# Kernel tuning notes

Hardware: AMD Instinct MI355X
Metric: run time of the kernel (lower is better)

Reference implementation:

```python
import jax, jax.numpy as jnp
import numpy as np

N_NODES = 100000
N_EDGES = 640000
D_FEAT = 128
IN_DIM = 4 + 2 * D_FEAT  # 260
HID = 128
OUT = 128


def setup_inputs() -> dict:
    key = jax.random.key(0)
    ks = jax.random.split(key, 6)
    x = jax.random.normal(ks[0], (N_NODES, D_FEAT), dtype=jnp.float32)
    edge_attr = jax.random.normal(ks[1], (N_EDGES, 4), dtype=jnp.float32)
    edge_index = jax.random.randint(ks[2], (2, N_EDGES), 0, N_NODES, dtype=jnp.int64)
    W1 = jax.random.normal(ks[3], (IN_DIM, HID), dtype=jnp.float32) * (1.0 / np.sqrt(IN_DIM))
    b1 = jnp.zeros((HID,), dtype=jnp.float32)
    W2 = jax.random.normal(ks[4], (HID, OUT), dtype=jnp.float32) * (1.0 / np.sqrt(HID))
    b2 = jnp.zeros((OUT,), dtype=jnp.float32)
    return {"x": x, "edge_attr": edge_attr, "edge_index": edge_index,
            "W1": W1, "b1": b1, "W2": W2, "b2": b2}


def reference(x, edge_attr, edge_index, W1, b1, W2, b2):
    # Gather sender/receiver node features via edge_index: [E, D]
    sender = x[edge_index[0]]
    receiver = x[edge_index[1]]
    # edge_attr already has 4 columns (matches the size-4 check in the torch code)
    edge_inputs = jnp.concatenate([edge_attr, sender, receiver], axis=1)  # [E, 4+2D]
    h = jax.nn.relu(edge_inputs @ W1 + b1)  # [E, HID]
    edge_attr_new = h @ W2 + b2             # [E, OUT]
    return edge_attr_new
```

## Files before the change

### kernel.cpp

```cpp
#include <hip/hip_runtime.h>
#include <hip/hip_bf16.h>

typedef __attribute__((ext_vector_type(4))) float f32x4;
typedef __attribute__((ext_vector_type(8))) short bf16x8;

typedef __attribute__((address_space(1))) unsigned int g_u32;
typedef __attribute__((address_space(3))) unsigned int l_u32;

__device__ __forceinline__ unsigned short f2bf(float f) {
  union { float f; unsigned int u; } v; v.f = f;
  unsigned int u = v.u;
  unsigned int r = (u + 0x7FFFu + ((u >> 16) & 1u)) >> 16;
  return (unsigned short)r;
}

__global__ void pack_w_kernel(const float* __restrict__ W1, const float* __restrict__ W2,
                              unsigned short* __restrict__ Bp1, unsigned short* __restrict__ Bp2) {
  int p = blockIdx.x * 256 + threadIdx.x;
  if (p < 32768) {
    int j = p & 7, n = (p >> 3) & 127, kb = p >> 10;
    Bp1[p] = f2bf(W1[(4 + kb * 8 + j) * 128 + n]);
  } else if (p < 49152) {
    int q = p - 32768;
    int j = q & 7, n = (q >> 3) & 127, kb = q >> 10;
    Bp2[q] = f2bf(W2[(kb * 8 + j) * 128 + n]);
  }
}

__global__ void convert_x_kernel(const float* __restrict__ x, unsigned short* __restrict__ xb, int n8) {
  int i = blockIdx.x * blockDim.x + threadIdx.x;
  if (i >= n8) return;
  const float4* s = (const float4*)x + (size_t)i * 2;
  float4 a = s[0], b = s[1];
  unsigned short h[8] = {f2bf(a.x), f2bf(a.y), f2bf(a.z), f2bf(a.w),
                         f2bf(b.x), f2bf(b.y), f2bf(b.z), f2bf(b.w)};
  int4 pk; __builtin_memcpy(&pk, h, 16);
  ((int4*)xb)[i] = pk;
}

constexpr int BM = 64;

template <bool XBF>
__global__ __launch_bounds__(256, 3)
void edge_main(const float* __restrict__ xf, const unsigned short* __restrict__ xb,
               const float* __restrict__ ea, const int* __restrict__ eidx,
               const float* __restrict__ W1, const float* __restrict__ b1,
               const float* __restrict__ b2,
               const unsigned short* __restrict__ Bp1, const unsigned short* __restrict__ Bp2,
               float* __restrict__ outp, int E) {
  __shared__ int4 AldsV[2048];
  __shared__ int4 HldsV[1024];
  __shared__ float ealds[256];

  char* Alds = (char*)AldsV;
  char* Hlds = (char*)HldsV;

  const int tid  = threadIdx.x;
  const int lane = tid & 63;
  const int wq   = lane >> 4;
  const int l16  = lane & 15;
  const int wave = tid >> 6;
  const int eb   = blockIdx.x * BM;

  ealds[tid] = ea[eb * 4 + tid];

  const int g  = tid & 15;
  const int s0 = tid >> 4;

  int idxv[8];
  #pragma unroll
  for (int it = 0; it < 8; ++it) {
    int seg = it * 16 + s0;
    idxv[it] = eidx[(seg & 1) * E + eb + (seg >> 1)];
  }

  const int c0 = wave * 32 + l16;
  const int c1 = c0 + 16;

  const float bias0 = b1[c0], bias1 = b1[c1];
  const float w00 = W1[c0],       w01 = W1[128 + c0], w02 = W1[256 + c0], w03 = W1[384 + c0];
  const float w10 = W1[c1],       w11 = W1[128 + c1], w12 = W1[256 + c1], w13 = W1[384 + c1];
  const float bias20 = b2[c0], bias21 = b2[c1];

  bf16x8 bf1r[8][2];
  #pragma unroll
  for (int ks = 0; ks < 8; ++ks) {
    int kb = ks * 4 + wq;
    bf1r[ks][0] = __builtin_bit_cast(bf16x8, *(const int4*)(Bp1 + ((size_t)kb * 128 + c0) * 8));
    bf1r[ks][1] = __builtin_bit_cast(bf16x8, *(const int4*)(Bp1 + ((size_t)kb * 128 + c1) * 8));
  }

  if (XBF) {
    #pragma unroll
    for (int it = 0; it < 8; ++it) {
      int seg = it * 16 + s0;
      int r = seg >> 1;
      int gs = g ^ (r & 7);
      const unsigned short* src = xb + (size_t)idxv[it] * 128 + gs * 8;
      char* dstbase = Alds + (it * 16 + wave * 4) * 256;
      __builtin_amdgcn_global_load_lds((g_u32*)(void*)src, (l_u32*)(void*)dstbase, 16, 0, 0);
    }
  } else {
    #pragma unroll
    for (int it = 0; it < 8; ++it) {
      int seg = it * 16 + s0;
      int r = seg >> 1, half = seg & 1;
      int idx = idxv[it];
      int lofs = (r * 512 + half * 256 + g * 16) ^ ((r & 7) << 4);
      const float* src = xf + (size_t)idx * 128 + g * 8;
      float4 a = *(const float4*)src;
      float4 c = *(const float4*)(src + 4);
      unsigned short h[8] = {f2bf(a.x), f2bf(a.y), f2bf(a.z), f2bf(a.w),
                             f2bf(c.x), f2bf(c.y), f2bf(c.z), f2bf(c.w)};
      int4 pk; __builtin_memcpy(&pk, h, 16);
      *(int4*)(Alds + lofs) = pk;
    }
  }
  __syncthreads();

  f32x4 acc[4][2];
  #pragma unroll
  for (int mf = 0; mf < 4; ++mf)
    #pragma unroll
    for (int rg = 0; rg < 4; ++rg) {
      int r = mf * 16 + wq * 4 + rg;
      float e0 = ealds[r * 4 + 0], e1 = ealds[r * 4 + 1];
      float e2 = ealds[r * 4 + 2], e3 = ealds[r * 4 + 3];
      acc[mf][0][rg] = bias0 + e0 * w00 + e1 * w01 + e2 * w02 + e3 * w03;
      acc[mf][1][rg] = bias1 + e0 * w10 + e1 * w11 + e2 * w12 + e3 * w13;
    }

  #pragma unroll
  for (int ks = 0; ks < 8; ++ks) {
    #pragma unroll
    for (int mf = 0; mf < 4; ++mf) {
      int r = mf * 16 + l16;
      int lofs = (r * 512 + ks * 64 + wq * 16) ^ ((r & 7) << 4);
      bf16x8 av = __builtin_bit_cast(bf16x8, *(const int4*)(Alds + lofs));
      acc[mf][0] = __builtin_amdgcn_mfma_f32_16x16x32_bf16(av, bf1r[ks][0], acc[mf][0], 0, 0, 0);
      acc[mf][1] = __builtin_amdgcn_mfma_f32_16x16x32_bf16(av, bf1r[ks][1], acc[mf][1], 0, 0, 0);
    }
  }

  bf16x8 bf2r[4][2];
  #pragma unroll
  for (int ks = 0; ks < 4; ++ks) {
    int kb = ks * 4 + wq;
    bf2r[ks][0] = __builtin_bit_cast(bf16x8, *(const int4*)(Bp2 + ((size_t)kb * 128 + c0) * 8));
    bf2r[ks][1] = __builtin_bit_cast(bf16x8, *(const int4*)(Bp2 + ((size_t)kb * 128 + c1) * 8));
  }

  #pragma unroll
  for (int mf = 0; mf < 4; ++mf)
    #pragma unroll
    for (int nf = 0; nf < 2; ++nf) {
      int c = wave * 32 + nf * 16 + l16;
      #pragma unroll
      for (int rg = 0; rg < 4; ++rg) {
        int r = mf * 16 + wq * 4 + rg;
        float v = fmaxf(acc[mf][nf][rg], 0.0f);
        int lofs = (r * 256 + c * 2) ^ ((r & 7) << 4);
        *(unsigned short*)(Hlds + lofs) = f2bf(v);
      }
    }
  __syncthreads();

  f32x4 acc2[4][2];
  #pragma unroll
  for (int mf = 0; mf < 4; ++mf) {
    acc2[mf][0] = (f32x4){bias20, bias20, bias20, bias20};
    acc2[mf][1] = (f32x4){bias21, bias21, bias21, bias21};
  }
  #pragma unroll
  for (int ks = 0; ks < 4; ++ks) {
    #pragma unroll
    for (int mf = 0; mf < 4; ++mf) {
      int r = mf * 16 + l16;
      int lofs = (r * 256 + ks * 64 + wq * 16) ^ ((r & 7) << 4);
      bf16x8 av = __builtin_bit_cast(bf16x8, *(const int4*)(Hlds + lofs));
      acc2[mf][0] = __builtin_amdgcn_mfma_f32_16x16x32_bf16(av, bf2r[ks][0], acc2[mf][0], 0, 0, 0);
      acc2[mf][1] = __builtin_amdgcn_mfma_f32_16x16x32_bf16(av, bf2r[ks][1], acc2[mf][1], 0, 0, 0);
    }
  }

  #pragma unroll
  for (int mf = 0; mf < 4; ++mf)
    #pragma unroll
    for (int nf = 0; nf < 2; ++nf) {
      int c = wave * 32 + nf * 16 + l16;
      #pragma unroll
      for (int rg = 0; rg < 4; ++rg) {
        int r = mf * 16 + wq * 4 + rg;
        outp[(size_t)(eb + r) * 128 + c] = acc2[mf][nf][rg];
      }
    }
}

extern "C" void kernel_launch(void* const* d_in, const int* in_sizes, int n_in,
                              void* d_out, int out_size, void* d_ws, size_t ws_size,
                              hipStream_t stream) {
  const float* x  = (const float*)d_in[0];
  const float* ea = (const float*)d_in[1];
  const int* eidx = (const int*)d_in[2];
  const float* W1 = (const float*)d_in[3];
  const float* b1 = (const float*)d_in[4];
  const float* W2 = (const float*)d_in[5];
  const float* b2 = (const float*)d_in[6];
  float* outp = (float*)d_out;

  const int E = in_sizes[2] / 2;
  const int nnodes = in_sizes[0] / 128;

  unsigned short* Bp1 = (unsigned short*)d_ws;
  unsigned short* Bp2 = Bp1 + 32768;
  unsigned short* xb  = (unsigned short*)((char*)d_ws + 98304);
  const size_t need = 98304 + (size_t)nnodes * 128 * 2;

  pack_w_kernel<<<192, 256, 0, stream>>>(W1, W2, Bp1, Bp2);

  if (ws_size >= need) {
    int n8 = nnodes * 128 / 8;
    convert_x_kernel<<<(n8 + 255) / 256, 256, 0, stream>>>(x, xb, n8);
    edge_main<true><<<E / BM, 256, 0, stream>>>(x, xb, ea, eidx, W1, b1, b2, Bp1, Bp2, outp, E);
  } else {
    edge_main<false><<<E / BM, 256, 0, stream>>>(x, xb, ea, eidx, W1, b1, b2, Bp1, Bp2, outp, E);
  }
}
```

Before: 156.5 us.

## Make edge MLP kernel persistent with prefetch of next tile's gather

Replaces the one-block-per-tile launch with a persistent grid of up to 768 blocks that loop over edge tiles. Each block keeps its W1 fragments in registers across tiles. It also issues the next tile's index loads, edge_attr loads and async global-to-LDS gathers while the current tile's second GEMM runs. Output stores become nontemporal. The aim is to hide gather latency and amortize per-block weight loading, at the cost of extra barriers and of LDS reuse that relies on explicit waitcnt ordering.

```diff
diff --git a/kernel.cpp b/kernel.cpp
--- a/kernel.cpp
+++ b/kernel.cpp
@@ -40,18 +40,192 @@
 
 constexpr int BM = 64;
 
-template <bool XBF>
 __global__ __launch_bounds__(256, 3)
-void edge_main(const float* __restrict__ xf, const unsigned short* __restrict__ xb,
-               const float* __restrict__ ea, const int* __restrict__ eidx,
-               const float* __restrict__ W1, const float* __restrict__ b1,
-               const float* __restrict__ b2,
-               const unsigned short* __restrict__ Bp1, const unsigned short* __restrict__ Bp2,
-               float* __restrict__ outp, int E) {
+void edge_persist(const unsigned short* __restrict__ xb,
+                  const float* __restrict__ ea, const int* __restrict__ eidx,
+                  const float* __restrict__ W1, const float* __restrict__ b1,
+                  const float* __restrict__ b2,
+                  const unsigned short* __restrict__ Bp1, const unsigned short* __restrict__ Bp2,
+                  float* __restrict__ outp, int E, int ntiles) {
+  __shared__ int4 AldsV[2048];
+  __shared__ int4 HldsV[1024];
+  __shared__ float ealds[2][256];
+
+  char* Alds = (char*)AldsV;
+  char* Hlds = (char*)HldsV;
+
+  const int tid  = threadIdx.x;
+  const int lane = tid & 63;
+  const int wq   = lane >> 4;
+  const int l16  = lane & 15;
+  const int wave = tid >> 6;
+  const int g    = tid & 15;
+  const int s0   = tid >> 4;
+
+  const int c0 = wave * 32 + l16;
+  const int c1 = c0 + 16;
+
+  const float bias0 = b1[c0], bias1 = b1[c1];
+  const float w00 = W1[c0],       w01 = W1[128 + c0], w02 = W1[256 + c0], w03 = W1[384 + c0];
+  const float w10 = W1[c1],       w11 = W1[128 + c1], w12 = W1[256 + c1], w13 = W1[384 + c1];
+  const float bias20 = b2[c0], bias21 = b2[c1];
+
+  bf16x8 bf1r[8][2];
+  #pragma unroll
+  for (int ks = 0; ks < 8; ++ks) {
+    int kb = ks * 4 + wq;
+    bf1r[ks][0] = __builtin_bit_cast(bf16x8, *(const int4*)(Bp1 + ((size_t)kb * 128 + c0) * 8));
+    bf1r[ks][1] = __builtin_bit_cast(bf16x8, *(const int4*)(Bp1 + ((size_t)kb * 128 + c1) * 8));
+  }
+
+  int tile = blockIdx.x;
+  if (tile >= ntiles) return;
+
+  {
+    int idx0[8];
+    #pragma unroll
+    for (int it = 0; it < 8; ++it) {
+      int seg = it * 16 + s0;
+      idx0[it] = eidx[(seg & 1) * E + tile * BM + (seg >> 1)];
+    }
+    ealds[0][tid] = ea[tile * 256 + tid];
+    #pragma unroll
+    for (int it = 0; it < 8; ++it) {
+      int seg = it * 16 + s0;
+      int r = seg >> 1;
+      int gs = g ^ (r & 7);
+      const unsigned short* src = xb + (size_t)idx0[it] * 128 + gs * 8;
+      char* dstbase = Alds + (it * 16 + wave * 4) * 256;
+      __builtin_amdgcn_global_load_lds((g_u32*)(void*)src, (l_u32*)(void*)dstbase, 16, 0, 0);
+    }
+  }
+
+  int p = 0;
+  for (; tile < ntiles; tile += gridDim.x) {
+    const int nt_ = tile + gridDim.x;
+    const int eb  = tile * BM;
+
+    asm volatile("s_waitcnt vmcnt(0) lgkmcnt(0)" ::: "memory");
+    __builtin_amdgcn_s_barrier();
+
+    int idxn[8];
+    if (nt_ < ntiles) {
+      #pragma unroll
+      for (int it = 0; it < 8; ++it) {
+        int seg = it * 16 + s0;
+        idxn[it] = eidx[(seg & 1) * E + nt_ * BM + (seg >> 1)];
+      }
+      ealds[p ^ 1][tid] = ea[nt_ * 256 + tid];
+    }
+
+    f32x4 acc[4][2];
+    #pragma unroll
+    for (int mf = 0; mf < 4; ++mf)
+      #pragma unroll
+      for (int rg = 0; rg < 4; ++rg) {
+        int r = mf * 16 + wq * 4 + rg;
+        float e0 = ealds[p][r * 4 + 0], e1 = ealds[p][r * 4 + 1];
+        float e2 = ealds[p][r * 4 + 2], e3 = ealds[p][r * 4 + 3];
+        acc[mf][0][rg] = bias0 + e0 * w00 + e1 * w01 + e2 * w02 + e3 * w03;
+        acc[mf][1][rg] = bias1 + e0 * w10 + e1 * w11 + e2 * w12 + e3 * w13;
+      }
+
+    #pragma unroll
+    for (int ks = 0; ks < 8; ++ks) {
+      #pragma unroll
+      for (int mf = 0; mf < 4; ++mf) {
+        int r = mf * 16 + l16;
+        int lofs = (r * 512 + ks * 64 + wq * 16) ^ ((r & 7) << 4);
+        bf16x8 av = __builtin_bit_cast(bf16x8, *(const int4*)(Alds + lofs));
+        acc[mf][0] = __builtin_amdgcn_mfma_f32_16x16x32_bf16(av, bf1r[ks][0], acc[mf][0], 0, 0, 0);
+        acc[mf][1] = __builtin_amdgcn_mfma_f32_16x16x32_bf16(av, bf1r[ks][1], acc[mf][1], 0, 0, 0);
+      }
+    }
+
+    asm volatile("s_waitcnt lgkmcnt(0)" ::: "memory");
+    __builtin_amdgcn_s_barrier();
+
+    if (nt_ < ntiles) {
+      #pragma unroll
+      for (int it = 0; it < 8; ++it) {
+        int seg = it * 16 + s0;
+        int r = seg >> 1;
+        int gs = g ^ (r & 7);
+        const unsigned short* src = xb + (size_t)idxn[it] * 128 + gs * 8;
+        char* dstbase = Alds + (it * 16 + wave * 4) * 256;
+        __builtin_amdgcn_global_load_lds((g_u32*)(void*)src, (l_u32*)(void*)dstbase, 16, 0, 0);
+      }
+    }
+
+    bf16x8 bf2r[4][2];
+    #pragma unroll
+    for (int ks = 0; ks < 4; ++ks) {
+      int kb = ks * 4 + wq;
+      bf2r[ks][0] = __builtin_bit_cast(bf16x8, *(const int4*)(Bp2 + ((size_t)kb * 128 + c0) * 8));
+      bf2r[ks][1] = __builtin_bit_cast(bf16x8, *(const int4*)(Bp2 + ((size_t)kb * 128 + c1) * 8));
+    }
+
+    #pragma unroll
+    for (int mf = 0; mf < 4; ++mf)
+      #pragma unroll
+      for (int nf = 0; nf < 2; ++nf) {
+        int c = wave * 32 + nf * 16 + l16;
+        #pragma unroll
+        for (int rg = 0; rg < 4; ++rg) {
+          int r = mf * 16 + wq * 4 + rg;
+          float v = fmaxf(acc[mf][nf][rg], 0.0f);
+          int lofs = (r * 256 + c * 2) ^ ((r & 7) << 4);
+          *(unsigned short*)(Hlds + lofs) = f2bf(v);
+        }
+      }
+
+    asm volatile("s_waitcnt lgkmcnt(0)" ::: "memory");
+    __builtin_amdgcn_s_barrier();
+
+    f32x4 acc2[4][2];
+    #pragma unroll
+    for (int mf = 0; mf < 4; ++mf) {
+      acc2[mf][0] = (f32x4){bias20, bias20, bias20, bias20};
+      acc2[mf][1] = (f32x4){bias21, bias21, bias21, bias21};
+    }
+    #pragma unroll
+    for (int ks = 0; ks < 4; ++ks) {
+      #pragma unroll
+      for (int mf = 0; mf < 4; ++mf) {
+        int r = mf * 16 + l16;
+        int lofs = (r * 256 + ks * 64 + wq * 16) ^ ((r & 7) << 4);
+        bf16x8 av = __builtin_bit_cast(bf16x8, *(const int4*)(Hlds + lofs));
+        acc2[mf][0] = __builtin_amdgcn_mfma_f32_16x16x32_bf16(av, bf2r[ks][0], acc2[mf][0], 0, 0, 0);
+        acc2[mf][1] = __builtin_amdgcn_mfma_f32_16x16x32_bf16(av, bf2r[ks][1], acc2[mf][1], 0, 0, 0);
+      }
+    }
+
+    #pragma unroll
+    for (int mf = 0; mf < 4; ++mf)
+      #pragma unroll
+      for (int nf = 0; nf < 2; ++nf) {
+        int c = wave * 32 + nf * 16 + l16;
+        #pragma unroll
+        for (int rg = 0; rg < 4; ++rg) {
+          int r = mf * 16 + wq * 4 + rg;
+          __builtin_nontemporal_store(acc2[mf][nf][rg], &outp[(size_t)(eb + r) * 128 + c]);
+        }
+      }
+
+    p ^= 1;
+  }
+}
+
+__global__ __launch_bounds__(256, 3)
+void edge_main_f32(const float* __restrict__ xf,
+                   const float* __restrict__ ea, const int* __restrict__ eidx,
+                   const float* __restrict__ W1, const float* __restrict__ b1,
+                   const float* __restrict__ b2,
+                   const unsigned short* __restrict__ Bp1, const unsigned short* __restrict__ Bp2,
+                   float* __restrict__ outp, int E) {
   __shared__ int4 AldsV[2048];
   __shared__ int4 HldsV[1024];
   __shared__ float ealds[256];
-
   char* Alds = (char*)AldsV;
   char* Hlds = (char*)HldsV;
 
@@ -76,7 +250,6 @@
 
   const int c0 = wave * 32 + l16;
   const int c1 = c0 + 16;
-
   const float bias0 = b1[c0], bias1 = b1[c1];
   const float w00 = W1[c0],       w01 = W1[128 + c0], w02 = W1[256 + c0], w03 = W1[384 + c0];
   const float w10 = W1[c1],       w11 = W1[128 + c1], w12 = W1[256 + c1], w13 = W1[384 + c1];
@@ -90,31 +263,18 @@
     bf1r[ks][1] = __builtin_bit_cast(bf16x8, *(const int4*)(Bp1 + ((size_t)kb * 128 + c1) * 8));
   }
 
-  if (XBF) {
-    #pragma unroll
-    for (int it = 0; it < 8; ++it) {
-      int seg = it * 16 + s0;
-      int r = seg >> 1;
-      int gs = g ^ (r & 7);
-      const unsigned short* src = xb + (size_t)idxv[it] * 128 + gs * 8;
-      char* dstbase = Alds + (it * 16 + wave * 4) * 256;
-      __builtin_amdgcn_global_load_lds((g_u32*)(void*)src, (l_u32*)(void*)dstbase, 16, 0, 0);
-    }
-  } else {
-    #pragma unroll
-    for (int it = 0; it < 8; ++it) {
-      int seg = it * 16 + s0;
-      int r = seg >> 1, half = seg & 1;
-      int idx = idxv[it];
-      int lofs = (r * 512 + half * 256 + g * 16) ^ ((r & 7) << 4);
-      const float* src = xf + (size_t)idx * 128 + g * 8;
-      float4 a = *(const float4*)src;
-      float4 c = *(const float4*)(src + 4);
-      unsigned short h[8] = {f2bf(a.x), f2bf(a.y), f2bf(a.z), f2bf(a.w),
-                             f2bf(c.x), f2bf(c.y), f2bf(c.z), f2bf(c.w)};
-      int4 pk; __builtin_memcpy(&pk, h, 16);
-      *(int4*)(Alds + lofs) = pk;
-    }
+  #pragma unroll
+  for (int it = 0; it < 8; ++it) {
+    int seg = it * 16 + s0;
+    int r = seg >> 1, half = seg & 1;
+    int lofs = (r * 512 + half * 256 + g * 16) ^ ((r & 7) << 4);
+    const float* src = xf + (size_t)idxv[it] * 128 + g * 8;
+    float4 a = *(const float4*)src;
+    float4 c = *(const float4*)(src + 4);
+    unsigned short h[8] = {f2bf(a.x), f2bf(a.y), f2bf(a.z), f2bf(a.w),
+                           f2bf(c.x), f2bf(c.y), f2bf(c.z), f2bf(c.w)};
+    int4 pk; __builtin_memcpy(&pk, h, 16);
+    *(int4*)(Alds + lofs) = pk;
   }
   __syncthreads();
 
@@ -131,7 +291,7 @@
     }
 
   #pragma unroll
-  for (int ks = 0; ks < 8; ++ks) {
+  for (int ks = 0; ks < 8; ++ks)
     #pragma unroll
     for (int mf = 0; mf < 4; ++mf) {
       int r = mf * 16 + l16;
@@ -140,7 +300,6 @@
       acc[mf][0] = __builtin_amdgcn_mfma_f32_16x16x32_bf16(av, bf1r[ks][0], acc[mf][0], 0, 0, 0);
       acc[mf][1] = __builtin_amdgcn_mfma_f32_16x16x32_bf16(av, bf1r[ks][1], acc[mf][1], 0, 0, 0);
     }
-  }
 
   bf16x8 bf2r[4][2];
   #pragma unroll
@@ -172,7 +331,7 @@
     acc2[mf][1] = (f32x4){bias21, bias21, bias21, bias21};
   }
   #pragma unroll
-  for (int ks = 0; ks < 4; ++ks) {
+  for (int ks = 0; ks < 4; ++ks)
     #pragma unroll
     for (int mf = 0; mf < 4; ++mf) {
       int r = mf * 16 + l16;
@@ -181,7 +340,6 @@
       acc2[mf][0] = __builtin_amdgcn_mfma_f32_16x16x32_bf16(av, bf2r[ks][0], acc2[mf][0], 0, 0, 0);
       acc2[mf][1] = __builtin_amdgcn_mfma_f32_16x16x32_bf16(av, bf2r[ks][1], acc2[mf][1], 0, 0, 0);
     }
-  }
 
   #pragma unroll
   for (int mf = 0; mf < 4; ++mf)
@@ -210,6 +368,7 @@
 
   const int E = in_sizes[2] / 2;
   const int nnodes = in_sizes[0] / 128;
+  const int ntiles = E / BM;
 
   unsigned short* Bp1 = (unsigned short*)d_ws;
   unsigned short* Bp2 = Bp1 + 32768;
@@ -221,8 +380,10 @@
   if (ws_size >= need) {
     int n8 = nnodes * 128 / 8;
     convert_x_kernel<<<(n8 + 255) / 256, 256, 0, stream>>>(x, xb, n8);
-    edge_main<true><<<E / BM, 256, 0, stream>>>(x, xb, ea, eidx, W1, b1, b2, Bp1, Bp2, outp, E);
+    int nblk = 768;
+    if (nblk > ntiles) nblk = ntiles;
+    edge_persist<<<nblk, 256, 0, stream>>>(xb, ea, eidx, W1, b1, b2, Bp1, Bp2, outp, E, ntiles);
   } else {
-    edge_main<false><<<E / BM, 256, 0, stream>>>(x, xb, ea, eidx, W1, b1, b2, Bp1, Bp2, outp, E);
-  }
-}
+    edge_main_f32<<<ntiles, 256, 0, stream>>>(x, ea, eidx, W1, b1, b2, Bp1, Bp2, outp, E);
+  }
+}
```

New measurement: 510.3 us. 226% more time.

## Swap MFMA operands to emit row-contiguous output and reuse LDS for hidden

Applied to the files above, without the earlier changes.

The bf16 fast path now puts the weight fragments in the A operand and the gathered edge features in B. Each lane therefore ends up holding four consecutive output features, so the second GEMM result is written with 16-byte vector stores and hidden activations are packed into 8-byte LDS stores. The hidden tile reuses the A buffer after an extra barrier, which drops the separate H buffer so launch bounds can ask for 4 blocks per CU. Bias and edge_attr weights are loaded as vectors. The cost is an additional __syncthreads and tighter register pressure at the higher occupancy target.

```diff
diff --git a/kernel.cpp b/kernel.cpp
--- a/kernel.cpp
+++ b/kernel.cpp
@@ -40,18 +40,162 @@
 
 constexpr int BM = 64;
 
-template <bool XBF>
-__global__ __launch_bounds__(256, 3)
-void edge_main(const float* __restrict__ xf, const unsigned short* __restrict__ xb,
+__global__ __launch_bounds__(256, 4)
+void edge_tile(const unsigned short* __restrict__ xb,
                const float* __restrict__ ea, const int* __restrict__ eidx,
                const float* __restrict__ W1, const float* __restrict__ b1,
                const float* __restrict__ b2,
                const unsigned short* __restrict__ Bp1, const unsigned short* __restrict__ Bp2,
                float* __restrict__ outp, int E) {
   __shared__ int4 AldsV[2048];
+  __shared__ float ealds[256];
+
+  char* Alds = (char*)AldsV;
+
+  const int tid  = threadIdx.x;
+  const int lane = tid & 63;
+  const int wq   = lane >> 4;
+  const int l16  = lane & 15;
+  const int wave = tid >> 6;
+  const int g    = tid & 15;
+  const int s0   = tid >> 4;
+  const int eb   = blockIdx.x * BM;
+
+  ealds[tid] = ea[eb * 4 + tid];
+
+  int idxv[8];
+  #pragma unroll
+  for (int it = 0; it < 8; ++it) {
+    int seg = it * 16 + s0;
+    idxv[it] = eidx[(seg & 1) * E + eb + (seg >> 1)];
+  }
+
+  const int f_lo0 = wave * 32 + wq * 4;
+  f32x4 b1v[2], b2v[2], w1v[2][4];
+  #pragma unroll
+  for (int fi = 0; fi < 2; ++fi) {
+    int f = f_lo0 + fi * 16;
+    b1v[fi] = *(const f32x4*)(b1 + f);
+    b2v[fi] = *(const f32x4*)(b2 + f);
+    #pragma unroll
+    for (int j = 0; j < 4; ++j)
+      w1v[fi][j] = *(const f32x4*)(W1 + j * 128 + f);
+  }
+
+  bf16x8 bf1r[8][2];
+  #pragma unroll
+  for (int ks = 0; ks < 8; ++ks) {
+    int kb = ks * 4 + wq;
+    #pragma unroll
+    for (int fi = 0; fi < 2; ++fi) {
+      int n = wave * 32 + fi * 16 + l16;
+      bf1r[ks][fi] = __builtin_bit_cast(bf16x8, *(const int4*)(Bp1 + ((size_t)kb * 128 + n) * 8));
+    }
+  }
+
+  #pragma unroll
+  for (int it = 0; it < 8; ++it) {
+    int seg = it * 16 + s0;
+    int r = seg >> 1;
+    int gs = g ^ (r & 7);
+    const unsigned short* src = xb + (size_t)idxv[it] * 128 + gs * 8;
+    char* dstbase = Alds + (it * 16 + wave * 4) * 256;
+    __builtin_amdgcn_global_load_lds((g_u32*)(void*)src, (l_u32*)(void*)dstbase, 16, 0, 0);
+  }
+  __syncthreads();
+
+  f32x4 acc[2][4];
+  #pragma unroll
+  for (int fi = 0; fi < 2; ++fi)
+    #pragma unroll
+    for (int et = 0; et < 4; ++et) {
+      int e = et * 16 + l16;
+      float e0 = ealds[e * 4 + 0], e1 = ealds[e * 4 + 1];
+      float e2 = ealds[e * 4 + 2], e3 = ealds[e * 4 + 3];
+      acc[fi][et] = b1v[fi] + e0 * w1v[fi][0] + e1 * w1v[fi][1]
+                            + e2 * w1v[fi][2] + e3 * w1v[fi][3];
+    }
+
+  #pragma unroll
+  for (int ks = 0; ks < 8; ++ks) {
+    #pragma unroll
+    for (int et = 0; et < 4; ++et) {
+      int e = et * 16 + l16;
+      int lofs = (e * 512 + ks * 64 + wq * 16) ^ ((e & 7) << 4);
+      bf16x8 av = __builtin_bit_cast(bf16x8, *(const int4*)(Alds + lofs));
+      acc[0][et] = __builtin_amdgcn_mfma_f32_16x16x32_bf16(bf1r[ks][0], av, acc[0][et], 0, 0, 0);
+      acc[1][et] = __builtin_amdgcn_mfma_f32_16x16x32_bf16(bf1r[ks][1], av, acc[1][et], 0, 0, 0);
+    }
+  }
+
+  bf16x8 bf2r[4][2];
+  #pragma unroll
+  for (int ks = 0; ks < 4; ++ks) {
+    int kb = ks * 4 + wq;
+    #pragma unroll
+    for (int fi = 0; fi < 2; ++fi) {
+      int n = wave * 32 + fi * 16 + l16;
+      bf2r[ks][fi] = __builtin_bit_cast(bf16x8, *(const int4*)(Bp2 + ((size_t)kb * 128 + n) * 8));
+    }
+  }
+
+  __syncthreads();
+
+  #pragma unroll
+  for (int fi = 0; fi < 2; ++fi)
+    #pragma unroll
+    for (int et = 0; et < 4; ++et) {
+      int e = et * 16 + l16;
+      float v0 = fmaxf(acc[fi][et][0], 0.0f);
+      float v1 = fmaxf(acc[fi][et][1], 0.0f);
+      float v2 = fmaxf(acc[fi][et][2], 0.0f);
+      float v3 = fmaxf(acc[fi][et][3], 0.0f);
+      uint2 pk;
+      pk.x = (unsigned int)f2bf(v0) | ((unsigned int)f2bf(v1) << 16);
+      pk.y = (unsigned int)f2bf(v2) | ((unsigned int)f2bf(v3) << 16);
+      int ho = (e * 256 + (wave * 32 + fi * 16 + wq * 4) * 2) ^ ((e & 7) << 4);
+      *(uint2*)(Alds + ho) = pk;
+    }
+
+  __syncthreads();
+
+  f32x4 acc2[2][4];
+  #pragma unroll
+  for (int fi = 0; fi < 2; ++fi)
+    #pragma unroll
+    for (int et = 0; et < 4; ++et)
+      acc2[fi][et] = b2v[fi];
+  #pragma unroll
+  for (int ks = 0; ks < 4; ++ks) {
+    #pragma unroll
+    for (int et = 0; et < 4; ++et) {
+      int e = et * 16 + l16;
+      int lofs = (e * 256 + ks * 64 + wq * 16) ^ ((e & 7) << 4);
+      bf16x8 hv = __builtin_bit_cast(bf16x8, *(const int4*)(Alds + lofs));
+      acc2[0][et] = __builtin_amdgcn_mfma_f32_16x16x32_bf16(bf2r[ks][0], hv, acc2[0][et], 0, 0, 0);
+      acc2[1][et] = __builtin_amdgcn_mfma_f32_16x16x32_bf16(bf2r[ks][1], hv, acc2[1][et], 0, 0, 0);
+    }
+  }
+
+  #pragma unroll
+  for (int fi = 0; fi < 2; ++fi)
+    #pragma unroll
+    for (int et = 0; et < 4; ++et) {
+      size_t row = (size_t)(eb + et * 16 + l16);
+      *(f32x4*)(outp + row * 128 + wave * 32 + fi * 16 + wq * 4) = acc2[fi][et];
+    }
+}
+
+__global__ __launch_bounds__(256, 3)
+void edge_main_f32(const float* __restrict__ xf,
+                   const float* __restrict__ ea, const int* __restrict__ eidx,
+                   const float* __restrict__ W1, const float* __restrict__ b1,
+                   const float* __restrict__ b2,
+                   const unsigned short* __restrict__ Bp1, const unsigned short* __restrict__ Bp2,
+                   float* __restrict__ outp, int E) {
+  __shared__ int4 AldsV[2048];
   __shared__ int4 HldsV[1024];
   __shared__ float ealds[256];
-
   char* Alds = (char*)AldsV;
   char* Hlds = (char*)HldsV;
 
@@ -76,7 +220,6 @@
 
   const int c0 = wave * 32 + l16;
   const int c1 = c0 + 16;
-
   const float bias0 = b1[c0], bias1 = b1[c1];
   const float w00 = W1[c0],       w01 = W1[128 + c0], w02 = W1[256 + c0], w03 = W1[384 + c0];
   const float w10 = W1[c1],       w11 = W1[128 + c1], w12 = W1[256 + c1], w13 = W1[384 + c1];
@@ -90,31 +233,18 @@
     bf1r[ks][1] = __builtin_bit_cast(bf16x8, *(const int4*)(Bp1 + ((size_t)kb * 128 + c1) * 8));
   }
 
-  if (XBF) {
-    #pragma unroll
-    for (int it = 0; it < 8; ++it) {
-      int seg = it * 16 + s0;
-      int r = seg >> 1;
-      int gs = g ^ (r & 7);
-      const unsigned short* src = xb + (size_t)idxv[it] * 128 + gs * 8;
-      char* dstbase = Alds + (it * 16 + wave * 4) * 256;
-      __builtin_amdgcn_global_load_lds((g_u32*)(void*)src, (l_u32*)(void*)dstbase, 16, 0, 0);
-    }
-  } else {
-    #pragma unroll
-    for (int it = 0; it < 8; ++it) {
-      int seg = it * 16 + s0;
-      int r = seg >> 1, half = seg & 1;
-      int idx = idxv[it];
-      int lofs = (r * 512 + half * 256 + g * 16) ^ ((r & 7) << 4);
-      const float* src = xf + (size_t)idx * 128 + g * 8;
-      float4 a = *(const float4*)src;
-      float4 c = *(const float4*)(src + 4);
-      unsigned short h[8] = {f2bf(a.x), f2bf(a.y), f2bf(a.z), f2bf(a.w),
-                             f2bf(c.x), f2bf(c.y), f2bf(c.z), f2bf(c.w)};
-      int4 pk; __builtin_memcpy(&pk, h, 16);
-      *(int4*)(Alds + lofs) = pk;
-    }
+  #pragma unroll
+  for (int it = 0; it < 8; ++it) {
+    int seg = it * 16 + s0;
+    int r = seg >> 1, half = seg & 1;
+    int lofs = (r * 512 + half * 256 + g * 16) ^ ((r & 7) << 4);
+    const float* src = xf + (size_t)idxv[it] * 128 + g * 8;
+    float4 a = *(const float4*)src;
+    float4 c = *(const float4*)(src + 4);
+    unsigned short h[8] = {f2bf(a.x), f2bf(a.y), f2bf(a.z), f2bf(a.w),
+                           f2bf(c.x), f2bf(c.y), f2bf(c.z), f2bf(c.w)};
+    int4 pk; __builtin_memcpy(&pk, h, 16);
+    *(int4*)(Alds + lofs) = pk;
   }
   __syncthreads();
 
@@ -131,7 +261,7 @@
     }
 
   #pragma unroll
-  for (int ks = 0; ks < 8; ++ks) {
+  for (int ks = 0; ks < 8; ++ks)
     #pragma unroll
     for (int mf = 0; mf < 4; ++mf) {
       int r = mf * 16 + l16;
@@ -140,7 +270,6 @@
       acc[mf][0] = __builtin_amdgcn_mfma_f32_16x16x32_bf16(av, bf1r[ks][0], acc[mf][0], 0, 0, 0);
       acc[mf][1] = __builtin_amdgcn_mfma_f32_16x16x32_bf16(av, bf1r[ks][1], acc[mf][1], 0, 0, 0);
     }
-  }
 
   bf16x8 bf2r[4][2];
   #pragma unroll
@@ -172,7 +301,7 @@
     acc2[mf][1] = (f32x4){bias21, bias21, bias21, bias21};
   }
   #pragma unroll
-  for (int ks = 0; ks < 4; ++ks) {
+  for (int ks = 0; ks < 4; ++ks)
     #pragma unroll
     for (int mf = 0; mf < 4; ++mf) {
       int r = mf * 16 + l16;
@@ -181,7 +310,6 @@
       acc2[mf][0] = __builtin_amdgcn_mfma_f32_16x16x32_bf16(av, bf2r[ks][0], acc2[mf][0], 0, 0, 0);
       acc2[mf][1] = __builtin_amdgcn_mfma_f32_16x16x32_bf16(av, bf2r[ks][1], acc2[mf][1], 0, 0, 0);
     }
-  }
 
   #pragma unroll
   for (int mf = 0; mf < 4; ++mf)
@@ -210,6 +338,7 @@
 
   const int E = in_sizes[2] / 2;
   const int nnodes = in_sizes[0] / 128;
+  const int ntiles = E / BM;
 
   unsigned short* Bp1 = (unsigned short*)d_ws;
   unsigned short* Bp2 = Bp1 + 32768;
@@ -221,8 +350,8 @@
   if (ws_size >= need) {
     int n8 = nnodes * 128 / 8;
     convert_x_kernel<<<(n8 + 255) / 256, 256, 0, stream>>>(x, xb, n8);
-    edge_main<true><<<E / BM, 256, 0, stream>>>(x, xb, ea, eidx, W1, b1, b2, Bp1, Bp2, outp, E);
+    edge_tile<<<ntiles, 256, 0, stream>>>(xb, ea, eidx, W1, b1, b2, Bp1, Bp2, outp, E);
   } else {
-    edge_main<false><<<E / BM, 256, 0, stream>>>(x, xb, ea, eidx, W1, b1, b2, Bp1, Bp2, outp, E);
-  }
-}
+    edge_main_f32<<<ntiles, 256, 0, stream>>>(x, ea, eidx, W1, b1, b2, Bp1, Bp2, outp, E);
+  }
+}
```

Measured after the change: 252.2 us. 61.1% more time.

## Drop bf16 pre-conversion of x and gather fp32 rows directly in main kernel

Applied to the files above, without the earlier changes.

Removes the separate convert_x kernel and the global-to-LDS bf16 gather path. The edge kernel now gathers fp32 node rows straight from x, issuing all the gather loads early into registers so they overlap with the weight-fragment loads, then converts to bf16 before writing to LDS. This saves one kernel launch and a full read/write pass over x. In exchange each gathered row moves twice as many bytes and needs more registers per thread.

```diff
diff --git a/kernel.cpp b/kernel.cpp
--- a/kernel.cpp
+++ b/kernel.cpp
@@ -3,9 +3,6 @@
 
 typedef __attribute__((ext_vector_type(4))) float f32x4;
 typedef __attribute__((ext_vector_type(8))) short bf16x8;
-
-typedef __attribute__((address_space(1))) unsigned int g_u32;
-typedef __attribute__((address_space(3))) unsigned int l_u32;
 
 __device__ __forceinline__ unsigned short f2bf(float f) {
   union { float f; unsigned int u; } v; v.f = f;
@@ -27,27 +24,15 @@
   }
 }
 
-__global__ void convert_x_kernel(const float* __restrict__ x, unsigned short* __restrict__ xb, int n8) {
-  int i = blockIdx.x * blockDim.x + threadIdx.x;
-  if (i >= n8) return;
-  const float4* s = (const float4*)x + (size_t)i * 2;
-  float4 a = s[0], b = s[1];
-  unsigned short h[8] = {f2bf(a.x), f2bf(a.y), f2bf(a.z), f2bf(a.w),
-                         f2bf(b.x), f2bf(b.y), f2bf(b.z), f2bf(b.w)};
-  int4 pk; __builtin_memcpy(&pk, h, 16);
-  ((int4*)xb)[i] = pk;
-}
-
 constexpr int BM = 64;
 
-template <bool XBF>
 __global__ __launch_bounds__(256, 3)
-void edge_main(const float* __restrict__ xf, const unsigned short* __restrict__ xb,
-               const float* __restrict__ ea, const int* __restrict__ eidx,
-               const float* __restrict__ W1, const float* __restrict__ b1,
-               const float* __restrict__ b2,
-               const unsigned short* __restrict__ Bp1, const unsigned short* __restrict__ Bp2,
-               float* __restrict__ outp, int E) {
+void edge_fused(const float* __restrict__ xf,
+                const float* __restrict__ ea, const int* __restrict__ eidx,
+                const float* __restrict__ W1, const float* __restrict__ b1,
+                const float* __restrict__ b2,
+                const unsigned short* __restrict__ Bp1, const unsigned short* __restrict__ Bp2,
+                float* __restrict__ outp, int E) {
   __shared__ int4 AldsV[2048];
   __shared__ int4 HldsV[1024];
   __shared__ float ealds[256];
@@ -60,18 +45,25 @@
   const int wq   = lane >> 4;
   const int l16  = lane & 15;
   const int wave = tid >> 6;
+  const int g    = tid & 15;
+  const int s0   = tid >> 4;
   const int eb   = blockIdx.x * BM;
 
   ealds[tid] = ea[eb * 4 + tid];
-
-  const int g  = tid & 15;
-  const int s0 = tid >> 4;
 
   int idxv[8];
   #pragma unroll
   for (int it = 0; it < 8; ++it) {
     int seg = it * 16 + s0;
     idxv[it] = eidx[(seg & 1) * E + eb + (seg >> 1)];
+  }
+
+  float4 ga[8], gb[8];
+  #pragma unroll
+  for (int it = 0; it < 8; ++it) {
+    const float* src = xf + (size_t)idxv[it] * 128 + g * 8;
+    ga[it] = *(const float4*)src;
+    gb[it] = *(const float4*)(src + 4);
   }
 
   const int c0 = wave * 32 + l16;
@@ -90,31 +82,15 @@
     bf1r[ks][1] = __builtin_bit_cast(bf16x8, *(const int4*)(Bp1 + ((size_t)kb * 128 + c1) * 8));
   }
 
-  if (XBF) {
-    #pragma unroll
-    for (int it = 0; it < 8; ++it) {
-      int seg = it * 16 + s0;
-      int r = seg >> 1;
-      int gs = g ^ (r & 7);
-      const unsigned short* src = xb + (size_t)idxv[it] * 128 + gs * 8;
-      char* dstbase = Alds + (it * 16 + wave * 4) * 256;
-      __builtin_amdgcn_global_load_lds((g_u32*)(void*)src, (l_u32*)(void*)dstbase, 16, 0, 0);
-    }
-  } else {
-    #pragma unroll
-    for (int it = 0; it < 8; ++it) {
-      int seg = it * 16 + s0;
-      int r = seg >> 1, half = seg & 1;
-      int idx = idxv[it];
-      int lofs = (r * 512 + half * 256 + g * 16) ^ ((r & 7) << 4);
-      const float* src = xf + (size_t)idx * 128 + g * 8;
-      float4 a = *(const float4*)src;
-      float4 c = *(const float4*)(src + 4);
-      unsigned short h[8] = {f2bf(a.x), f2bf(a.y), f2bf(a.z), f2bf(a.w),
-                             f2bf(c.x), f2bf(c.y), f2bf(c.z), f2bf(c.w)};
-      int4 pk; __builtin_memcpy(&pk, h, 16);
-      *(int4*)(Alds + lofs) = pk;
-    }
+  #pragma unroll
+  for (int it = 0; it < 8; ++it) {
+    int seg = it * 16 + s0;
+    int r = seg >> 1, half = seg & 1;
+    int lofs = (r * 512 + half * 256 + g * 16) ^ ((r & 7) << 4);
+    unsigned short h[8] = {f2bf(ga[it].x), f2bf(ga[it].y), f2bf(ga[it].z), f2bf(ga[it].w),
+                           f2bf(gb[it].x), f2bf(gb[it].y), f2bf(gb[it].z), f2bf(gb[it].w)};
+    int4 pk; __builtin_memcpy(&pk, h, 16);
+    *(int4*)(Alds + lofs) = pk;
   }
   __syncthreads();
 
@@ -209,20 +185,11 @@
   float* outp = (float*)d_out;
 
   const int E = in_sizes[2] / 2;
-  const int nnodes = in_sizes[0] / 128;
+  const int ntiles = E / BM;
 
   unsigned short* Bp1 = (unsigned short*)d_ws;
   unsigned short* Bp2 = Bp1 + 32768;
-  unsigned short* xb  = (unsigned short*)((char*)d_ws + 98304);
-  const size_t need = 98304 + (size_t)nnodes * 128 * 2;
 
   pack_w_kernel<<<192, 256, 0, stream>>>(W1, W2, Bp1, Bp2);
-
-  if (ws_size >= need) {
-    int n8 = nnodes * 128 / 8;
-    convert_x_kernel<<<(n8 + 255) / 256, 256, 0, stream>>>(x, xb, n8);
-    edge_main<true><<<E / BM, 256, 0, stream>>>(x, xb, ea, eidx, W1, b1, b2, Bp1, Bp2, outp, E);
-  } else {
-    edge_main<false><<<E / BM, 256, 0, stream>>>(x, xb, ea, eidx, W1, b1, b2, Bp1, Bp2, outp, E);
-  }
+  edge_fused<<<ntiles, 256, 0, stream>>>(x, ea, eidx, W1, b1, b2, Bp1, Bp2, outp, E);
 }
```

Measured after the change: 156.5 us. About the same (+0.0%).
